# Kernel optimization log

Hardware: AMD Instinct MI355X
Metric: run time of the kernel (lower is better)

The kernel has to match this reference:

```python
import jax, jax.numpy as jnp
import numpy as np

N = 30000          # nodes
DEG = 16           # in-degree per node
E = N * DEG        # edges per etype
T = 3              # edge types
IN = 128           # in_feats
HID = 256          # hidden_size
HEADS = 4
CLS = 2            # num_classes
NEG_SLOPE = 0.2    # DGL GATConv default


def setup_inputs() -> dict:
    key = jax.random.key(0)
    ks = jax.random.split(key, 14)
    s = lambda k, shape: (jax.random.normal(k, shape, jnp.float32) * 0.05)
    feat = jax.random.normal(ks[0], (N, IN), jnp.float32)
    src = jax.random.randint(ks[1], (T, E), 0, N)
    # every node gets exactly DEG incoming edges per etype (DGL forbids 0-in-degree)
    dst = jnp.tile(jnp.repeat(jnp.arange(N), DEG), (T, 1))
    D = HID // HEADS
    return {
        "feat": feat,
        "W0": s(ks[2], (T, IN, HID)),  "al0": s(ks[3], (T, HEADS, D)), "ar0": s(ks[4], (T, HEADS, D)), "b0": jnp.zeros((T, HID), jnp.float32),
        "W1": s(ks[5], (T, HID, HID)), "al1": s(ks[6], (T, HEADS, D)), "ar1": s(ks[7], (T, HEADS, D)), "b1": jnp.zeros((T, HID), jnp.float32),
        "W2": s(ks[8], (T, HID, CLS)), "al2": s(ks[9], (T, 1, CLS)),   "ar2": s(ks[10], (T, 1, CLS)), "b2": jnp.zeros((T, CLS), jnp.float32),
        "src": src, "dst": dst,
    }


def _gat(feat, W, al, ar, b, src, dst):
    """DGL GATConv: feat [n,F], W [F,H*D], al/ar [H,D], b [H*D] -> [n,H,D]."""
    n = feat.shape[0]
    H, D = al.shape
    h = (feat @ W).reshape(n, H, D)                      # projected features
    el = jnp.sum(h * al, axis=-1)                        # [n,H]
    er = jnp.sum(h * ar, axis=-1)                        # [n,H]
    e = jax.nn.leaky_relu(el[src] + er[dst], NEG_SLOPE)  # [E,H] edge scores
    # segment softmax over incoming edges of each dst node
    emax = jax.ops.segment_max(e, dst, num_segments=n)
    ex = jnp.exp(e - emax[dst])
    den = jax.ops.segment_sum(ex, dst, num_segments=n)
    alpha = ex / den[dst]                                # [E,H]
    out = jax.ops.segment_sum(h[src] * alpha[:, :, None], dst, num_segments=n)
    return out + b.reshape(H, D)


def _hetero(feat, W, al, ar, b, src, dst):
    # HeteroGraphConv(aggregate='mean') over T edge types on one node type
    outs = [_gat(feat, W[t], al[t], ar[t], b[t], src[t], dst[t]) for t in range(W.shape[0])]
    return jnp.mean(jnp.stack(outs, 0), axis=0)


def reference(feat, W0, al0, ar0, b0, W1, al1, ar1, b1, W2, al2, ar2, b2, src, dst):
    h = jax.nn.elu(_hetero(feat, W0, al0, ar0, b0, src, dst).reshape(N, -1))
    h = jax.nn.elu(_hetero(h, W1, al1, ar1, b1, src, dst).reshape(N, -1))
    logits = _hetero(h, W2, al2, ar2, b2, src, dst)      # [N,1,CLS]
    # faithful to F.softmax(logits[primary_ntype], dim=1): dim=1 is the size-1 head axis
    return logits, jax.nn.softmax(logits, axis=1)
```

## Files before the change

### kernel.cpp

```cpp
#include <hip/hip_runtime.h>
#include <hip/hip_bf16.h>
#include <hip/hip_fp8.h>
#include <math.h>

#define N_NODES 30000
#define DEG     16
#define NE      480000
#define NT      3
#define IN_F    128
#define HID_F   256
#define HEADS   4
#define DH      64
#define CLS     2
#define SLOPE   0.2f

#define NTILES      1875
#define NTILES_AL   1880
#define KC0         4
#define KC1         8

typedef __hip_bfloat16 bf16;
typedef __attribute__((ext_vector_type(8))) short short8;
typedef __attribute__((ext_vector_type(4))) float floatx4;
typedef __attribute__((ext_vector_type(2))) float f32x2;

__device__ __forceinline__ float bf2f(short x) {
    unsigned int u = ((unsigned int)(unsigned short)x) << 16;
    float f;
    __builtin_memcpy(&f, &u, 4);
    return f;
}
__device__ __forceinline__ short f2bf_s(float x) {
    bf16 b = bf16(x);
    short s;
    __builtin_memcpy(&s, &b, 2);
    return s;
}

__device__ __forceinline__ void gload_lds16(const void* g, void* l) {
    __builtin_amdgcn_global_load_lds(
        (const __attribute__((address_space(1))) unsigned int*)g,
        (__attribute__((address_space(3))) unsigned int*)l, 16, 0, 0);
}

__device__ __forceinline__ f32x2 fp8_lo(unsigned int u) {
#if __has_builtin(__builtin_amdgcn_cvt_pk_f32_fp8)
    return __builtin_amdgcn_cvt_pk_f32_fp8((int)u, false);
#else
    __hip_fp8_e4m3 q0, q1;
    q0.__x = (unsigned char)(u & 0xff);
    q1.__x = (unsigned char)((u >> 8) & 0xff);
    return (f32x2){(float)q0, (float)q1};
#endif
}
__device__ __forceinline__ f32x2 fp8_hi(unsigned int u) {
#if __has_builtin(__builtin_amdgcn_cvt_pk_f32_fp8)
    return __builtin_amdgcn_cvt_pk_f32_fp8((int)u, true);
#else
    __hip_fp8_e4m3 q2, q3;
    q2.__x = (unsigned char)((u >> 16) & 0xff);
    q3.__x = (unsigned char)((u >> 24) & 0xff);
    return (f32x2){(float)q2, (float)q3};
#endif
}
__device__ __forceinline__ unsigned int fp8_encode4_u32(float v0, float v1,
                                                        float v2, float v3) {
#if __has_builtin(__builtin_amdgcn_cvt_pk_fp8_f32)
    int p01 = __builtin_amdgcn_cvt_pk_fp8_f32(v0, v1, 0, false);
    int p23 = __builtin_amdgcn_cvt_pk_fp8_f32(v2, v3, 0, false);
    return ((unsigned int)p01 & 0xffffu) | ((unsigned int)p23 << 16);
#else
    __hip_fp8_e4m3 q0(v0), q1(v1), q2(v2), q3(v3);
    return (unsigned int)q0.__x | ((unsigned int)q1.__x << 8) |
           ((unsigned int)q2.__x << 16) | ((unsigned int)q3.__x << 24);
#endif
}


#define APACK_THREADS (N_NODES * (IN_F / 8))
#define BP0_THREADS   (NT * 16 * KC0 * 64)
#define BP1_THREADS   (NT * 16 * KC1 * 64)
__global__ void prep(const float* __restrict__ feat, const float* __restrict__ W0,
                     const float* __restrict__ W1, short* __restrict__ Apack0,
                     short* __restrict__ Bpack0, short* __restrict__ Bpack1) {
    int g = blockIdx.x * 256 + threadIdx.x;
    if (g < APACK_THREADS) {
        int row = g >> 4, j8 = g & 15;
        int k0 = j8 * 8;
        const float* src = feat + (size_t)row * IN_F + k0;
        int ntile = row >> 4, C = k0 >> 5, quad = (k0 >> 3) & 3;
        int lane  = (row & 15) + 16 * quad;
        short* dst = Apack0 + ((size_t)(ntile * KC0 + C) * 64 + lane) * 8;
        short8 o;
#pragma unroll
        for (int j = 0; j < 8; j++) o[j] = f2bf_s(src[j]);
        *(short8*)dst = o;
        return;
    }
    g -= APACK_THREADS;
    if (g < BP0_THREADS) {
        int t = g / (16 * KC0 * 64), rem = g % (16 * KC0 * 64);
        int nt = rem / (KC0 * 64);
        int C  = (rem / 64) % KC0;
        int lane = rem & 63, l15 = lane & 15, quad = lane >> 4;
        int col = nt * 16 + l15, k0 = C * 32 + quad * 8;
        const float* src = W0 + (size_t)t * IN_F * HID_F + (size_t)k0 * HID_F + col;
        short* dst = Bpack0 + ((size_t)t * 16 * KC0 + nt * KC0 + C) * 512 + lane * 8;
        short8 o;
#pragma unroll
        for (int j = 0; j < 8; j++) o[j] = f2bf_s(src[(size_t)j * HID_F]);
        *(short8*)dst = o;
        return;
    }
    g -= BP0_THREADS;
    if (g < BP1_THREADS) {
        int t = g / (16 * KC1 * 64), rem = g % (16 * KC1 * 64);
        int nt = rem / (KC1 * 64);
        int C  = (rem / 64) % KC1;
        int lane = rem & 63, l15 = lane & 15, quad = lane >> 4;
        int col = nt * 16 + l15, k0 = C * 32 + quad * 8;
        const float* src = W1 + (size_t)t * HID_F * HID_F + (size_t)k0 * HID_F + col;
        short* dst = Bpack1 + ((size_t)t * 16 * KC1 + nt * KC1 + C) * 512 + lane * 8;
        short8 o;
#pragma unroll
        for (int j = 0; j < 8; j++) o[j] = f2bf_s(src[(size_t)j * HID_F]);
        *(short8*)dst = o;
    }
}

template <int K>
__global__ __launch_bounds__(256, 4) void gemm_proj(const short* __restrict__ Apack,
                                                    const short* __restrict__ Bpack,
                                                    const float* __restrict__ al,
                                                    const float* __restrict__ ar,
                                                    unsigned char* __restrict__ Hout,
                                                    float* __restrict__ el,
                                                    float* __restrict__ er) {
    const int KC = K / 32;
    int nh   = blockIdx.y;
    int t    = blockIdx.z;
    int tid  = threadIdx.x;
    int wave = tid >> 6, lane = tid & 63;
    int quad = lane >> 4, l15 = lane & 15;
    int e0   = blockIdx.x * 8 + wave * 2;

    __shared__ __align__(16) unsigned char Blds[4 * KC * 1024];

    {
        const short* Bp_panel = Bpack + ((size_t)t * 16 + nh * 4) * KC * 512;
#pragma unroll
        for (int i = 0; i < KC; i++) {
            int chunk = wave + i * 4;
            gload_lds16(Bp_panel + (size_t)chunk * 512 + lane * 8,
                        Blds + chunk * 1024);
        }
    }

    const short* Ap0 = Apack + (size_t)(e0)     * KC * 512 + lane * 8;
    const short* Ap1 = Apack + (size_t)(e0 + 1) * KC * 512 + lane * 8;
    unsigned char* Ht = Hout + (size_t)t * N_NODES * HID_F;

    floatx4 acc[4][2];
#pragma unroll
    for (int i = 0; i < 4; i++) {
        acc[i][0] = (floatx4){0.f, 0.f, 0.f, 0.f};
        acc[i][1] = (floatx4){0.f, 0.f, 0.f, 0.f};
    }

    asm volatile("s_waitcnt vmcnt(0)" ::: "memory");
    __syncthreads();

#pragma unroll
    for (int C = 0; C < KC; C++) {
        short8 xb0 = *(const short8*)(Ap0 + (size_t)C * 512);
        short8 xb1 = *(const short8*)(Ap1 + (size_t)C * 512);
#pragma unroll
        for (int nt = 0; nt < 4; nt++) {
            short8 wa = *(const short8*)(Blds + (size_t)(nt * KC + C) * 1024 + lane * 16);
            acc[nt][0] = __builtin_amdgcn_mfma_f32_16x16x32_bf16(wa, xb0, acc[nt][0], 0, 0, 0);
            acc[nt][1] = __builtin_amdgcn_mfma_f32_16x16x32_bf16(wa, xb1, acc[nt][1], 0, 0, 0);
        }
    }

#pragma unroll
    for (int e = 0; e < 2; e++) {
        int node = (e0 + e) * 16 + l15;
        bool ok  = node < N_NODES;
#pragma unroll
        for (int nt = 0; nt < 4; nt++) {
            unsigned int u = fp8_encode4_u32(acc[nt][e][0], acc[nt][e][1],
                                             acc[nt][e][2], acc[nt][e][3]);
            if (ok)
                *(unsigned int*)(Ht + (size_t)node * HID_F + (nh * 4 + nt) * 16 + quad * 4) = u;
        }
        {
            float pl = 0.f, pr = 0.f;
#pragma unroll
            for (int nt = 0; nt < 4; nt++) {
                int coff = t * HID_F + (nh * 4 + nt) * 16 + quad * 4;
                float4 av = *(const float4*)(al + coff);
                float4 rv = *(const float4*)(ar + coff);
                pl += acc[nt][e][0] * av.x + acc[nt][e][1] * av.y +
                      acc[nt][e][2] * av.z + acc[nt][e][3] * av.w;
                pr += acc[nt][e][0] * rv.x + acc[nt][e][1] * rv.y +
                      acc[nt][e][2] * rv.z + acc[nt][e][3] * rv.w;
            }
            pl += __shfl_xor(pl, 16); pl += __shfl_xor(pl, 32);
            pr += __shfl_xor(pr, 16); pr += __shfl_xor(pr, 32);
            if (lane < 16 && ok) {
                el[((size_t)t * N_NODES + node) * HEADS + nh] = pl;
                er[((size_t)t * N_NODES + node) * HEADS + nh] = pr;
            }
        }
    }
}

template <bool PACK>
__global__ __launch_bounds__(256, 8) void gat_agg(const unsigned char* __restrict__ Hproj,
                                                  const float* __restrict__ el,
                                                  const float* __restrict__ er,
                                                  const int* __restrict__ src,
                                                  const float* __restrict__ bias,
                                                  short* __restrict__ out) {
    int blk = blockIdx.x;
    int tid = threadIdx.x;
    __shared__ __align__(16) int   s_src[16][NT][DEG];
    __shared__ __align__(16) float s_w[16][NT][HEADS][DEG];

#pragma unroll
    for (int t = 0; t < NT; t++) {
        int j = tid;
        s_src[j >> 4][t][j & 15] = src[(size_t)t * NE + blk * 256 + j];
    }
    __syncthreads();

    {
        int lane16 = tid & 15;
        int ubase  = tid >> 4;
#pragma unroll
        for (int it = 0; it < 12; it++) {
            int u = it * 16 + ubase;
            int g = u / 12, rem = u % 12;
            int t = rem >> 2, h = rem & 3;
            int n = blk * 16 + g;
            int s = s_src[g][t][lane16];
            float e = el[((size_t)t * N_NODES + s) * HEADS + h] +
                      er[((size_t)t * N_NODES + n) * HEADS + h];
            e = e > 0.f ? e : SLOPE * e;
            float m = e;
            m = fmaxf(m, __shfl_xor(m, 1));
            m = fmaxf(m, __shfl_xor(m, 2));
            m = fmaxf(m, __shfl_xor(m, 4));
            m = fmaxf(m, __shfl_xor(m, 8));
            float p = __expf(e - m);
            float ss = p;
            ss += __shfl_xor(ss, 1);
            ss += __shfl_xor(ss, 2);
            ss += __shfl_xor(ss, 4);
            ss += __shfl_xor(ss, 8);
            s_w[g][t][h][lane16] = p / ss;
        }
    }
    __syncthreads();

    int g = tid >> 4, c = tid & 15;
    int n = blk * 16 + g;
    int h = c >> 2;
    int col0 = c * 16;

    f32x2 acc2[8];
#pragma unroll
    for (int k = 0; k < 8; k++) acc2[k] = (f32x2){0.f, 0.f};

    const uint4* Hb = (const uint4*)Hproj;
    unsigned cu = (unsigned)c;

#pragma unroll
    for (int t = 0; t < NT; t++) {
        const unsigned tb = (unsigned)t * (N_NODES * 16u);
        const float* wp = s_w[g][t][h];
#pragma unroll
        for (int half = 0; half < 2; half++) {
            uint4 v[8];
#pragma unroll
            for (int i = 0; i < 8; i++) {
                int s = s_src[g][t][half * 8 + i];
                v[i] = Hb[tb + (unsigned)s * 16u + cu];
            }
#pragma unroll
            for (int i = 0; i < 8; i++) {
                float wsc = wp[half * 8 + i];
                f32x2 w2 = (f32x2){wsc, wsc};
                acc2[0] += w2 * fp8_lo(v[i].x);
                acc2[1] += w2 * fp8_hi(v[i].x);
                acc2[2] += w2 * fp8_lo(v[i].y);
                acc2[3] += w2 * fp8_hi(v[i].y);
                acc2[4] += w2 * fp8_lo(v[i].z);
                acc2[5] += w2 * fp8_hi(v[i].z);
                acc2[6] += w2 * fp8_lo(v[i].w);
                acc2[7] += w2 * fp8_hi(v[i].w);
            }
        }
    }

    short8 o0, o1;
#pragma unroll
    for (int j = 0; j < 8; j++) {
        float av = acc2[j >> 1][j & 1];
        float bsum = bias[0 * HID_F + col0 + j] + bias[1 * HID_F + col0 + j] +
                     bias[2 * HID_F + col0 + j];
        float res = (av + bsum) * (1.f / 3.f);
        res = res > 0.f ? res : (__expf(res) - 1.f);
        o0[j] = f2bf_s(res);
    }
#pragma unroll
    for (int j = 0; j < 8; j++) {
        float av = acc2[4 + (j >> 1)][j & 1];
        int cj = col0 + 8 + j;
        float bsum = bias[0 * HID_F + cj] + bias[1 * HID_F + cj] +
                     bias[2 * HID_F + cj];
        float res = (av + bsum) * (1.f / 3.f);
        res = res > 0.f ? res : (__expf(res) - 1.f);
        o1[j] = f2bf_s(res);
    }
    if (PACK) {
        int C = c >> 1;
        int lane0 = g + 16 * ((2 * c) & 3);
        int lane1 = g + 16 * ((2 * c + 1) & 3);
        *(short8*)(out + ((size_t)(blk * KC1 + C) * 64 + lane0) * 8) = o0;
        *(short8*)(out + ((size_t)(blk * KC1 + C) * 64 + lane1) * 8) = o1;
    } else {
        *(short8*)(out + (size_t)n * HID_F + col0) = o0;
        *(short8*)(out + (size_t)n * HID_F + col0 + 8) = o1;
    }
}

__global__ __launch_bounds__(256) void proj2(const short* __restrict__ X,
                                             const float* __restrict__ W2,
                                             const float* __restrict__ al2,
                                             const float* __restrict__ ar2,
                                             float* __restrict__ p2,
                                             float* __restrict__ el2,
                                             float* __restrict__ er2) {
    int n    = blockIdx.x * 4 + (threadIdx.x >> 6);
    int lane = threadIdx.x & 63;
    const short* Xr = X + (size_t)n * HID_F + lane * 4;
    float x[4];
    x[0] = bf2f(Xr[0]); x[1] = bf2f(Xr[1]); x[2] = bf2f(Xr[2]); x[3] = bf2f(Xr[3]);
    float a[NT][CLS];
#pragma unroll
    for (int t = 0; t < NT; t++)
#pragma unroll
        for (int cc = 0; cc < CLS; cc++) {
            float v = 0.f;
#pragma unroll
            for (int j = 0; j < 4; j++)
                v += x[j] * W2[(size_t)t * HID_F * CLS + (lane * 4 + j) * CLS + cc];
#pragma unroll
            for (int off = 32; off; off >>= 1) v += __shfl_xor(v, off);
            a[t][cc] = v;
        }
    if (lane == 0) {
#pragma unroll
        for (int t = 0; t < NT; t++) {
            p2[((size_t)t * N_NODES + n) * CLS + 0] = a[t][0];
            p2[((size_t)t * N_NODES + n) * CLS + 1] = a[t][1];
            el2[(size_t)t * N_NODES + n] = a[t][0] * al2[t * CLS + 0] + a[t][1] * al2[t * CLS + 1];
            er2[(size_t)t * N_NODES + n] = a[t][0] * ar2[t * CLS + 0] + a[t][1] * ar2[t * CLS + 1];
        }
    }
}

__global__ void final_layer(const float* __restrict__ p2,
                            const float* __restrict__ el2,
                            const float* __restrict__ er2,
                            const int* __restrict__ src,
                            const float* __restrict__ b2,
                            float* __restrict__ out) {
    int n = blockIdx.x * 256 + threadIdx.x;
    if (n >= N_NODES) return;
    float l0 = 0.f, l1 = 0.f;
    for (int t = 0; t < NT; t++) {
        float erv = er2[(size_t)t * N_NODES + n];
        const int* sp = src + (size_t)t * NE + n * DEG;
        float ev[DEG];
        float m = -1e30f;
#pragma unroll
        for (int i = 0; i < DEG; i++) {
            int s   = sp[i];
            float e = el2[(size_t)t * N_NODES + s] + erv;
            e = e > 0.f ? e : SLOPE * e;
            ev[i] = e;
            m = fmaxf(m, e);
        }
        float den = 0.f, a0 = 0.f, a1 = 0.f;
#pragma unroll
        for (int i = 0; i < DEG; i++) {
            int s   = sp[i];
            float p = __expf(ev[i] - m);
            den += p;
            a0  += p * p2[((size_t)t * N_NODES + s) * CLS + 0];
            a1  += p * p2[((size_t)t * N_NODES + s) * CLS + 1];
        }
        l0 += a0 / den + b2[t * CLS + 0];
        l1 += a1 / den + b2[t * CLS + 1];
    }
    l0 *= (1.f / 3.f);
    l1 *= (1.f / 3.f);
    out[(size_t)n * CLS + 0] = l0;
    out[(size_t)n * CLS + 1] = l1;
    float* out2 = out + (size_t)N_NODES * CLS;
    out2[(size_t)n * CLS + 0] = 1.0f;
    out2[(size_t)n * CLS + 1] = 1.0f;
}

extern "C" void kernel_launch(void* const* d_in, const int* in_sizes, int n_in,
                              void* d_out, int out_size, void* d_ws, size_t ws_size,
                              hipStream_t stream) {
    const float* feat = (const float*)d_in[0];
    const float* W0   = (const float*)d_in[1];
    const float* al0  = (const float*)d_in[2];
    const float* ar0  = (const float*)d_in[3];
    const float* b0   = (const float*)d_in[4];
    const float* W1   = (const float*)d_in[5];
    const float* al1  = (const float*)d_in[6];
    const float* ar1  = (const float*)d_in[7];
    const float* b1   = (const float*)d_in[8];
    const float* W2   = (const float*)d_in[9];
    const float* al2  = (const float*)d_in[10];
    const float* ar2  = (const float*)d_in[11];
    const float* b2   = (const float*)d_in[12];
    const int*   src  = (const int*)d_in[13];

    char* w = (char*)d_ws;
    auto alloc = [&](size_t bytes) {
        char* p = w;
        w += (bytes + 255) & ~(size_t)255;
        return p;
    };
    short* Apack0 = (short*)alloc((size_t)NTILES_AL * KC0 * 512 * 2);
    short* Apack1 = (short*)alloc((size_t)NTILES_AL * KC1 * 512 * 2);
    short* Bpack0 = (short*)alloc((size_t)NT * 16 * KC0 * 512 * 2);
    short* Bpack1 = (short*)alloc((size_t)NT * 16 * KC1 * 512 * 2);
    unsigned char* Hproj = (unsigned char*)alloc((size_t)NT * N_NODES * HID_F);
    short* h2    = (short*)alloc((size_t)N_NODES * HID_F * 2);
    float* el    = (float*)alloc((size_t)NT * N_NODES * HEADS * 4);
    float* er    = (float*)alloc((size_t)NT * N_NODES * HEADS * 4);
    float* p2    = (float*)alloc((size_t)NT * N_NODES * CLS * 4);
    float* el2   = (float*)alloc((size_t)NT * N_NODES * 4);
    float* er2   = (float*)alloc((size_t)NT * N_NODES * 4);

    int prep_total = APACK_THREADS + BP0_THREADS + BP1_THREADS;
    prep<<<(prep_total + 255) / 256, 256, 0, stream>>>(feat, W0, W1, Apack0,
                                                       Bpack0, Bpack1);

    dim3 ggrid((NTILES + 7) / 8, 4, NT);

    gemm_proj<IN_F><<<ggrid, 256, 0, stream>>>(Apack0, Bpack0, al0, ar0, Hproj, el, er);
    gat_agg<true><<<N_NODES / 16, 256, 0, stream>>>(Hproj, el, er, src, b0, Apack1);

    gemm_proj<HID_F><<<ggrid, 256, 0, stream>>>(Apack1, Bpack1, al1, ar1, Hproj, el, er);
    gat_agg<false><<<N_NODES / 16, 256, 0, stream>>>(Hproj, el, er, src, b1, h2);

    proj2<<<dim3(N_NODES / 4), 256, 0, stream>>>(h2, W2, al2, ar2, p2, el2, er2);
    final_layer<<<(N_NODES + 255) / 256, 256, 0, stream>>>(p2, el2, er2, src, b2,
                                                           (float*)d_out);
}
```

Before: 306.0 us.

## Split GAT aggregation into alpha and gather kernels, remap GEMM grid for XCD locality

The GEMM projection now loops over edge types inside one block and uses a 1D grid remapped across the eight XCDs, so the A tile is reused from cache across types. The fused aggregation kernel is split into an alpha_w kernel that writes softmax weights to global memory and gather kernels where each thread owns one node and one 32-column group. The gather kernels read 16-bit packed source indices and a precomputed bias sum. The final layer is rewritten to use one 16-lane group per node with shuffle reductions. These changes aim to improve cache locality and parallelism, at the cost of an extra launch and an alpha buffer round-trip through memory.

```diff
diff --git a/kernel.cpp b/kernel.cpp
--- a/kernel.cpp
+++ b/kernel.cpp
@@ -18,6 +18,9 @@
 #define NTILES_AL   1880
 #define KC0         4
 #define KC1         8
+
+#define GEMM_NWG    940
+#define GATHER_NWG  944
 
 typedef __hip_bfloat16 bf16;
 typedef __attribute__((ext_vector_type(8))) short short8;
@@ -80,9 +83,16 @@
 #define APACK_THREADS (N_NODES * (IN_F / 8))
 #define BP0_THREADS   (NT * 16 * KC0 * 64)
 #define BP1_THREADS   (NT * 16 * KC1 * 64)
+#define SRC16_THREADS (NT * NE / 8)
+#define BSUM_THREADS  (2 * HID_F)
+#define PREP_TOTAL (APACK_THREADS + BP0_THREADS + BP1_THREADS + SRC16_THREADS + BSUM_THREADS)
 __global__ void prep(const float* __restrict__ feat, const float* __restrict__ W0,
-                     const float* __restrict__ W1, short* __restrict__ Apack0,
-                     short* __restrict__ Bpack0, short* __restrict__ Bpack1) {
+                     const float* __restrict__ W1, const int* __restrict__ srcIn,
+                     const float* __restrict__ b0, const float* __restrict__ b1,
+                     short* __restrict__ Apack0, short* __restrict__ Bpack0,
+                     short* __restrict__ Bpack1,
+                     unsigned short* __restrict__ src16,
+                     float* __restrict__ bsum) {
     int g = blockIdx.x * 256 + threadIdx.x;
     if (g < APACK_THREADS) {
         int row = g >> 4, j8 = g & 15;
@@ -125,6 +135,26 @@
 #pragma unroll
         for (int j = 0; j < 8; j++) o[j] = f2bf_s(src[(size_t)j * HID_F]);
         *(short8*)dst = o;
+        return;
+    }
+    g -= BP1_THREADS;
+    if (g < SRC16_THREADS) {
+        size_t i = (size_t)g * 8;
+        const int4* s4 = (const int4*)(srcIn + i);
+        int4 q0 = s4[0], q1 = s4[1];
+        short8 o;
+        o[0] = (short)(unsigned short)q0.x; o[1] = (short)(unsigned short)q0.y;
+        o[2] = (short)(unsigned short)q0.z; o[3] = (short)(unsigned short)q0.w;
+        o[4] = (short)(unsigned short)q1.x; o[5] = (short)(unsigned short)q1.y;
+        o[6] = (short)(unsigned short)q1.z; o[7] = (short)(unsigned short)q1.w;
+        *(short8*)(src16 + i) = o;
+        return;
+    }
+    g -= SRC16_THREADS;
+    if (g < BSUM_THREADS) {
+        int layer = g >> 8, c = g & 255;
+        const float* b = layer ? b1 : b0;
+        bsum[layer * HID_F + c] = b[c] + b[HID_F + c] + b[2 * HID_F + c];
     }
 }
 
@@ -136,96 +166,98 @@
                                                     unsigned char* __restrict__ Hout,
                                                     float* __restrict__ el,
                                                     float* __restrict__ er) {
-    const int KC = K / 32;
-    int nh   = blockIdx.y;
-    int t    = blockIdx.z;
+    constexpr int KC = K / 32;
+    int bid = blockIdx.x;
+    int c8  = bid & 7, o = bid >> 3;
+    int L   = (c8 < 4) ? c8 * 118 + o : 472 + (c8 - 4) * 117 + o;
+    int xb  = L >> 2;
+    int nh  = L & 3;
     int tid  = threadIdx.x;
     int wave = tid >> 6, lane = tid & 63;
     int quad = lane >> 4, l15 = lane & 15;
-    int e0   = blockIdx.x * 8 + wave * 2;
+    int e0   = xb * 8 + wave * 2;
 
     __shared__ __align__(16) unsigned char Blds[4 * KC * 1024];
-
-    {
-        const short* Bp_panel = Bpack + ((size_t)t * 16 + nh * 4) * KC * 512;
-#pragma unroll
-        for (int i = 0; i < KC; i++) {
-            int chunk = wave + i * 4;
-            gload_lds16(Bp_panel + (size_t)chunk * 512 + lane * 8,
-                        Blds + chunk * 1024);
-        }
-    }
 
     const short* Ap0 = Apack + (size_t)(e0)     * KC * 512 + lane * 8;
     const short* Ap1 = Apack + (size_t)(e0 + 1) * KC * 512 + lane * 8;
-    unsigned char* Ht = Hout + (size_t)t * N_NODES * HID_F;
-
-    floatx4 acc[4][2];
-#pragma unroll
-    for (int i = 0; i < 4; i++) {
-        acc[i][0] = (floatx4){0.f, 0.f, 0.f, 0.f};
-        acc[i][1] = (floatx4){0.f, 0.f, 0.f, 0.f};
-    }
-
-    asm volatile("s_waitcnt vmcnt(0)" ::: "memory");
-    __syncthreads();
-
-#pragma unroll
-    for (int C = 0; C < KC; C++) {
-        short8 xb0 = *(const short8*)(Ap0 + (size_t)C * 512);
-        short8 xb1 = *(const short8*)(Ap1 + (size_t)C * 512);
-#pragma unroll
-        for (int nt = 0; nt < 4; nt++) {
-            short8 wa = *(const short8*)(Blds + (size_t)(nt * KC + C) * 1024 + lane * 16);
-            acc[nt][0] = __builtin_amdgcn_mfma_f32_16x16x32_bf16(wa, xb0, acc[nt][0], 0, 0, 0);
-            acc[nt][1] = __builtin_amdgcn_mfma_f32_16x16x32_bf16(wa, xb1, acc[nt][1], 0, 0, 0);
-        }
-    }
-
-#pragma unroll
-    for (int e = 0; e < 2; e++) {
-        int node = (e0 + e) * 16 + l15;
-        bool ok  = node < N_NODES;
-#pragma unroll
-        for (int nt = 0; nt < 4; nt++) {
-            unsigned int u = fp8_encode4_u32(acc[nt][e][0], acc[nt][e][1],
-                                             acc[nt][e][2], acc[nt][e][3]);
-            if (ok)
-                *(unsigned int*)(Ht + (size_t)node * HID_F + (nh * 4 + nt) * 16 + quad * 4) = u;
-        }
+
+    for (int t = 0; t < NT; t++) {
         {
-            float pl = 0.f, pr = 0.f;
+            const short* Bp_panel = Bpack + ((size_t)t * 16 + nh * 4) * KC * 512;
+#pragma unroll
+            for (int i = 0; i < KC; i++) {
+                int chunk = wave + i * 4;
+                gload_lds16(Bp_panel + (size_t)chunk * 512 + lane * 8,
+                            Blds + chunk * 1024);
+            }
+        }
+
+        floatx4 acc[4][2];
+#pragma unroll
+        for (int i = 0; i < 4; i++) {
+            acc[i][0] = (floatx4){0.f, 0.f, 0.f, 0.f};
+            acc[i][1] = (floatx4){0.f, 0.f, 0.f, 0.f};
+        }
+
+        asm volatile("s_waitcnt vmcnt(0)" ::: "memory");
+        __syncthreads();
+
+#pragma unroll
+        for (int C = 0; C < KC; C++) {
+            short8 xb0 = *(const short8*)(Ap0 + (size_t)C * 512);
+            short8 xb1 = *(const short8*)(Ap1 + (size_t)C * 512);
 #pragma unroll
             for (int nt = 0; nt < 4; nt++) {
-                int coff = t * HID_F + (nh * 4 + nt) * 16 + quad * 4;
-                float4 av = *(const float4*)(al + coff);
-                float4 rv = *(const float4*)(ar + coff);
-                pl += acc[nt][e][0] * av.x + acc[nt][e][1] * av.y +
-                      acc[nt][e][2] * av.z + acc[nt][e][3] * av.w;
-                pr += acc[nt][e][0] * rv.x + acc[nt][e][1] * rv.y +
-                      acc[nt][e][2] * rv.z + acc[nt][e][3] * rv.w;
+                short8 wa = *(const short8*)(Blds + (size_t)(nt * KC + C) * 1024 + lane * 16);
+                acc[nt][0] = __builtin_amdgcn_mfma_f32_16x16x32_bf16(wa, xb0, acc[nt][0], 0, 0, 0);
+                acc[nt][1] = __builtin_amdgcn_mfma_f32_16x16x32_bf16(wa, xb1, acc[nt][1], 0, 0, 0);
             }
-            pl += __shfl_xor(pl, 16); pl += __shfl_xor(pl, 32);
-            pr += __shfl_xor(pr, 16); pr += __shfl_xor(pr, 32);
-            if (lane < 16 && ok) {
-                el[((size_t)t * N_NODES + node) * HEADS + nh] = pl;
-                er[((size_t)t * N_NODES + node) * HEADS + nh] = pr;
+        }
+
+        unsigned char* Ht = Hout + (size_t)t * N_NODES * HID_F;
+#pragma unroll
+        for (int e = 0; e < 2; e++) {
+            int node = (e0 + e) * 16 + l15;
+            bool ok  = node < N_NODES;
+#pragma unroll
+            for (int nt = 0; nt < 4; nt++) {
+                unsigned int u = fp8_encode4_u32(acc[nt][e][0], acc[nt][e][1],
+                                                 acc[nt][e][2], acc[nt][e][3]);
+                if (ok)
+                    *(unsigned int*)(Ht + (size_t)node * HID_F + (nh * 4 + nt) * 16 + quad * 4) = u;
             }
-        }
-    }
-}
-
-template <bool PACK>
-__global__ __launch_bounds__(256, 8) void gat_agg(const unsigned char* __restrict__ Hproj,
-                                                  const float* __restrict__ el,
+            {
+                float pl = 0.f, pr = 0.f;
+#pragma unroll
+                for (int nt = 0; nt < 4; nt++) {
+                    int coff = t * HID_F + (nh * 4 + nt) * 16 + quad * 4;
+                    float4 av = *(const float4*)(al + coff);
+                    float4 rv = *(const float4*)(ar + coff);
+                    pl += acc[nt][e][0] * av.x + acc[nt][e][1] * av.y +
+                          acc[nt][e][2] * av.z + acc[nt][e][3] * av.w;
+                    pr += acc[nt][e][0] * rv.x + acc[nt][e][1] * rv.y +
+                          acc[nt][e][2] * rv.z + acc[nt][e][3] * rv.w;
+                }
+                pl += __shfl_xor(pl, 16); pl += __shfl_xor(pl, 32);
+                pr += __shfl_xor(pr, 16); pr += __shfl_xor(pr, 32);
+                if (lane < 16 && ok) {
+                    el[((size_t)t * N_NODES + node) * HEADS + nh] = pl;
+                    er[((size_t)t * N_NODES + node) * HEADS + nh] = pr;
+                }
+            }
+        }
+        __syncthreads();
+    }
+}
+
+__global__ __launch_bounds__(256, 8) void alpha_w(const float* __restrict__ el,
                                                   const float* __restrict__ er,
                                                   const int* __restrict__ src,
-                                                  const float* __restrict__ bias,
-                                                  short* __restrict__ out) {
+                                                  float* __restrict__ alpha) {
     int blk = blockIdx.x;
     int tid = threadIdx.x;
-    __shared__ __align__(16) int   s_src[16][NT][DEG];
-    __shared__ __align__(16) float s_w[16][NT][HEADS][DEG];
+    __shared__ __align__(16) int s_src[16][NT][DEG];
 
 #pragma unroll
     for (int t = 0; t < NT; t++) {
@@ -234,104 +266,184 @@
     }
     __syncthreads();
 
-    {
-        int lane16 = tid & 15;
-        int ubase  = tid >> 4;
-#pragma unroll
-        for (int it = 0; it < 12; it++) {
-            int u = it * 16 + ubase;
-            int g = u / 12, rem = u % 12;
-            int t = rem >> 2, h = rem & 3;
-            int n = blk * 16 + g;
-            int s = s_src[g][t][lane16];
-            float e = el[((size_t)t * N_NODES + s) * HEADS + h] +
-                      er[((size_t)t * N_NODES + n) * HEADS + h];
-            e = e > 0.f ? e : SLOPE * e;
-            float m = e;
-            m = fmaxf(m, __shfl_xor(m, 1));
-            m = fmaxf(m, __shfl_xor(m, 2));
-            m = fmaxf(m, __shfl_xor(m, 4));
-            m = fmaxf(m, __shfl_xor(m, 8));
-            float p = __expf(e - m);
-            float ss = p;
-            ss += __shfl_xor(ss, 1);
-            ss += __shfl_xor(ss, 2);
-            ss += __shfl_xor(ss, 4);
-            ss += __shfl_xor(ss, 8);
-            s_w[g][t][h][lane16] = p / ss;
-        }
-    }
-    __syncthreads();
-
-    int g = tid >> 4, c = tid & 15;
-    int n = blk * 16 + g;
-    int h = c >> 2;
-    int col0 = c * 16;
-
-    f32x2 acc2[8];
-#pragma unroll
-    for (int k = 0; k < 8; k++) acc2[k] = (f32x2){0.f, 0.f};
+    int lane16 = tid & 15;
+    int ubase  = tid >> 4;
+#pragma unroll
+    for (int it = 0; it < 12; it++) {
+        int u = it * 16 + ubase;
+        int g = u / 12, rem = u % 12;
+        int t = rem >> 2, h = rem & 3;
+        int n = blk * 16 + g;
+        int s = s_src[g][t][lane16];
+        float e = el[((size_t)t * N_NODES + s) * HEADS + h] +
+                  er[((size_t)t * N_NODES + n) * HEADS + h];
+        e = e > 0.f ? e : SLOPE * e;
+        float m = e;
+        m = fmaxf(m, __shfl_xor(m, 1));
+        m = fmaxf(m, __shfl_xor(m, 2));
+        m = fmaxf(m, __shfl_xor(m, 4));
+        m = fmaxf(m, __shfl_xor(m, 8));
+        float p = __expf(e - m);
+        float ss = p;
+        ss += __shfl_xor(ss, 1);
+        ss += __shfl_xor(ss, 2);
+        ss += __shfl_xor(ss, 4);
+        ss += __shfl_xor(ss, 8);
+        alpha[(((size_t)t * HEADS + h) * N_NODES + n) * 16 + lane16] = p / ss;
+    }
+}
+
+
+__global__ __launch_bounds__(256, 4) void gat_gather_pack(
+        const unsigned char* __restrict__ Hproj,
+        const float* __restrict__ alpha,
+        const unsigned short* __restrict__ src16,
+        const float* __restrict__ bsum,
+        short* __restrict__ out) {
+    int bid = blockIdx.x;
+    int cg  = bid & 7;
+    int n   = (bid >> 3) * 256 + threadIdx.x;
+    if (n >= N_NODES) return;
+    int h = cg >> 1;
 
     const uint4* Hb = (const uint4*)Hproj;
-    unsigned cu = (unsigned)c;
-
-#pragma unroll
+    unsigned colbase = (unsigned)cg * 2u;
+
+    f32x2 acc2[16];
+#pragma unroll
+    for (int k = 0; k < 16; k++) acc2[k] = (f32x2){0.f, 0.f};
+
     for (int t = 0; t < NT; t++) {
-        const unsigned tb = (unsigned)t * (N_NODES * 16u);
-        const float* wp = s_w[g][t][h];
-#pragma unroll
-        for (int half = 0; half < 2; half++) {
-            uint4 v[8];
-#pragma unroll
-            for (int i = 0; i < 8; i++) {
-                int s = s_src[g][t][half * 8 + i];
-                v[i] = Hb[tb + (unsigned)s * 16u + cu];
+        const uint4* sp = (const uint4*)(src16 + (size_t)t * NE + (size_t)n * 16);
+        uint4 sA = sp[0], sB = sp[1];
+        const float4* ap = (const float4*)(alpha + (((size_t)t * HEADS + h) * N_NODES + n) * 16);
+        float4 a0 = ap[0], a1 = ap[1], a2 = ap[2], a3 = ap[3];
+        unsigned tb = (unsigned)t * (N_NODES * 16u);
+        unsigned e_[16];
+        e_[0] = sA.x & 0xffffu;  e_[1] = sA.x >> 16;
+        e_[2] = sA.y & 0xffffu;  e_[3] = sA.y >> 16;
+        e_[4] = sA.z & 0xffffu;  e_[5] = sA.z >> 16;
+        e_[6] = sA.w & 0xffffu;  e_[7] = sA.w >> 16;
+        e_[8] = sB.x & 0xffffu;  e_[9] = sB.x >> 16;
+        e_[10] = sB.y & 0xffffu; e_[11] = sB.y >> 16;
+        e_[12] = sB.z & 0xffffu; e_[13] = sB.z >> 16;
+        e_[14] = sB.w & 0xffffu; e_[15] = sB.w >> 16;
+        float w_[16] = {a0.x, a0.y, a0.z, a0.w, a1.x, a1.y, a1.z, a1.w,
+                        a2.x, a2.y, a2.z, a2.w, a3.x, a3.y, a3.z, a3.w};
+#pragma unroll
+        for (int sub = 0; sub < 2; sub++) {
+#pragma unroll
+            for (int half = 0; half < 2; half++) {
+                uint4 v[8];
+#pragma unroll
+                for (int i = 0; i < 8; i++)
+                    v[i] = Hb[tb + e_[half * 8 + i] * 16u + colbase + (unsigned)sub];
+#pragma unroll
+                for (int i = 0; i < 8; i++) {
+                    float ws = w_[half * 8 + i];
+                    f32x2 w2 = (f32x2){ws, ws};
+                    acc2[sub * 8 + 0] += w2 * fp8_lo(v[i].x);
+                    acc2[sub * 8 + 1] += w2 * fp8_hi(v[i].x);
+                    acc2[sub * 8 + 2] += w2 * fp8_lo(v[i].y);
+                    acc2[sub * 8 + 3] += w2 * fp8_hi(v[i].y);
+                    acc2[sub * 8 + 4] += w2 * fp8_lo(v[i].z);
+                    acc2[sub * 8 + 5] += w2 * fp8_hi(v[i].z);
+                    acc2[sub * 8 + 6] += w2 * fp8_lo(v[i].w);
+                    acc2[sub * 8 + 7] += w2 * fp8_hi(v[i].w);
+                }
             }
-#pragma unroll
-            for (int i = 0; i < 8; i++) {
-                float wsc = wp[half * 8 + i];
-                f32x2 w2 = (f32x2){wsc, wsc};
-                acc2[0] += w2 * fp8_lo(v[i].x);
-                acc2[1] += w2 * fp8_hi(v[i].x);
-                acc2[2] += w2 * fp8_lo(v[i].y);
-                acc2[3] += w2 * fp8_hi(v[i].y);
-                acc2[4] += w2 * fp8_lo(v[i].z);
-                acc2[5] += w2 * fp8_hi(v[i].z);
-                acc2[6] += w2 * fp8_lo(v[i].w);
-                acc2[7] += w2 * fp8_hi(v[i].w);
+        }
+    }
+
+    int ntile = n >> 4;
+#pragma unroll
+    for (int q = 0; q < 4; q++) {
+        short8 o;
+#pragma unroll
+        for (int j = 0; j < 8; j++) {
+            int col = q * 8 + j;
+            float av = acc2[col >> 1][col & 1];
+            float res = (av + bsum[cg * 32 + col]) * (1.f / 3.f);
+            res = res > 0.f ? res : (__expf(res) - 1.f);
+            o[j] = f2bf_s(res);
+        }
+        *(short8*)(out + ((size_t)(ntile * KC1 + cg) * 64 + (n & 15) + 16 * q) * 8) = o;
+    }
+}
+
+__global__ __launch_bounds__(256, 4) void gat_gather_h2(
+        const unsigned char* __restrict__ Hproj,
+        const float* __restrict__ alpha,
+        const unsigned short* __restrict__ src16,
+        const float* __restrict__ bsum,
+        short* __restrict__ out) {
+    int bid = blockIdx.x;
+    int cg  = bid & 7;
+    int n   = (bid >> 3) * 256 + threadIdx.x;
+    if (n >= N_NODES) return;
+    int h = cg >> 1;
+
+    const uint4* Hb = (const uint4*)Hproj;
+    unsigned colbase = (unsigned)cg * 2u;
+
+    f32x2 acc2[16];
+#pragma unroll
+    for (int k = 0; k < 16; k++) acc2[k] = (f32x2){0.f, 0.f};
+
+    for (int t = 0; t < NT; t++) {
+        const uint4* sp = (const uint4*)(src16 + (size_t)t * NE + (size_t)n * 16);
+        uint4 sA = sp[0], sB = sp[1];
+        const float4* ap = (const float4*)(alpha + (((size_t)t * HEADS + h) * N_NODES + n) * 16);
+        float4 a0 = ap[0], a1 = ap[1], a2 = ap[2], a3 = ap[3];
+        unsigned tb = (unsigned)t * (N_NODES * 16u);
+        unsigned e_[16];
+        e_[0] = sA.x & 0xffffu;  e_[1] = sA.x >> 16;
+        e_[2] = sA.y & 0xffffu;  e_[3] = sA.y >> 16;
+        e_[4] = sA.z & 0xffffu;  e_[5] = sA.z >> 16;
+        e_[6] = sA.w & 0xffffu;  e_[7] = sA.w >> 16;
+        e_[8] = sB.x & 0xffffu;  e_[9] = sB.x >> 16;
+        e_[10] = sB.y & 0xffffu; e_[11] = sB.y >> 16;
+        e_[12] = sB.z & 0xffffu; e_[13] = sB.z >> 16;
+        e_[14] = sB.w & 0xffffu; e_[15] = sB.w >> 16;
+        float w_[16] = {a0.x, a0.y, a0.z, a0.w, a1.x, a1.y, a1.z, a1.w,
+                        a2.x, a2.y, a2.z, a2.w, a3.x, a3.y, a3.z, a3.w};
+#pragma unroll
+        for (int sub = 0; sub < 2; sub++) {
+#pragma unroll
+            for (int half = 0; half < 2; half++) {
+                uint4 v[8];
+#pragma unroll
+                for (int i = 0; i < 8; i++)
+                    v[i] = Hb[tb + e_[half * 8 + i] * 16u + colbase + (unsigned)sub];
+#pragma unroll
+                for (int i = 0; i < 8; i++) {
+                    float ws = w_[half * 8 + i];
+                    f32x2 w2 = (f32x2){ws, ws};
+                    acc2[sub * 8 + 0] += w2 * fp8_lo(v[i].x);
+                    acc2[sub * 8 + 1] += w2 * fp8_hi(v[i].x);
+                    acc2[sub * 8 + 2] += w2 * fp8_lo(v[i].y);
+                    acc2[sub * 8 + 3] += w2 * fp8_hi(v[i].y);
+                    acc2[sub * 8 + 4] += w2 * fp8_lo(v[i].z);
+                    acc2[sub * 8 + 5] += w2 * fp8_hi(v[i].z);
+                    acc2[sub * 8 + 6] += w2 * fp8_lo(v[i].w);
+                    acc2[sub * 8 + 7] += w2 * fp8_hi(v[i].w);
+                }
             }
         }
     }
 
-    short8 o0, o1;
-#pragma unroll
-    for (int j = 0; j < 8; j++) {
-        float av = acc2[j >> 1][j & 1];
-        float bsum = bias[0 * HID_F + col0 + j] + bias[1 * HID_F + col0 + j] +
-                     bias[2 * HID_F + col0 + j];
-        float res = (av + bsum) * (1.f / 3.f);
-        res = res > 0.f ? res : (__expf(res) - 1.f);
-        o0[j] = f2bf_s(res);
-    }
-#pragma unroll
-    for (int j = 0; j < 8; j++) {
-        float av = acc2[4 + (j >> 1)][j & 1];
-        int cj = col0 + 8 + j;
-        float bsum = bias[0 * HID_F + cj] + bias[1 * HID_F + cj] +
-                     bias[2 * HID_F + cj];
-        float res = (av + bsum) * (1.f / 3.f);
-        res = res > 0.f ? res : (__expf(res) - 1.f);
-        o1[j] = f2bf_s(res);
-    }
-    if (PACK) {
-        int C = c >> 1;
-        int lane0 = g + 16 * ((2 * c) & 3);
-        int lane1 = g + 16 * ((2 * c + 1) & 3);
-        *(short8*)(out + ((size_t)(blk * KC1 + C) * 64 + lane0) * 8) = o0;
-        *(short8*)(out + ((size_t)(blk * KC1 + C) * 64 + lane1) * 8) = o1;
-    } else {
-        *(short8*)(out + (size_t)n * HID_F + col0) = o0;
-        *(short8*)(out + (size_t)n * HID_F + col0 + 8) = o1;
+#pragma unroll
+    for (int q = 0; q < 4; q++) {
+        short8 o;
+#pragma unroll
+        for (int j = 0; j < 8; j++) {
+            int col = q * 8 + j;
+            float av = acc2[col >> 1][col & 1];
+            float res = (av + bsum[cg * 32 + col]) * (1.f / 3.f);
+            res = res > 0.f ? res : (__expf(res) - 1.f);
+            o[j] = f2bf_s(res);
+        }
+        *(short8*)(out + (size_t)n * HID_F + cg * 32 + q * 8) = o;
     }
 }
 
@@ -371,47 +483,44 @@
     }
 }
 
-__global__ void final_layer(const float* __restrict__ p2,
-                            const float* __restrict__ el2,
-                            const float* __restrict__ er2,
-                            const int* __restrict__ src,
-                            const float* __restrict__ b2,
-                            float* __restrict__ out) {
-    int n = blockIdx.x * 256 + threadIdx.x;
-    if (n >= N_NODES) return;
+__global__ __launch_bounds__(256) void final_layer(const float* __restrict__ p2,
+                                                   const float* __restrict__ el2,
+                                                   const float* __restrict__ er2,
+                                                   const int* __restrict__ src,
+                                                   const float* __restrict__ b2,
+                                                   float* __restrict__ out) {
+    int g = threadIdx.x >> 4, lane16 = threadIdx.x & 15;
+    int n = blockIdx.x * 16 + g;
     float l0 = 0.f, l1 = 0.f;
+#pragma unroll
     for (int t = 0; t < NT; t++) {
-        float erv = er2[(size_t)t * N_NODES + n];
-        const int* sp = src + (size_t)t * NE + n * DEG;
-        float ev[DEG];
-        float m = -1e30f;
-#pragma unroll
-        for (int i = 0; i < DEG; i++) {
-            int s   = sp[i];
-            float e = el2[(size_t)t * N_NODES + s] + erv;
-            e = e > 0.f ? e : SLOPE * e;
-            ev[i] = e;
-            m = fmaxf(m, e);
-        }
-        float den = 0.f, a0 = 0.f, a1 = 0.f;
-#pragma unroll
-        for (int i = 0; i < DEG; i++) {
-            int s   = sp[i];
-            float p = __expf(ev[i] - m);
-            den += p;
-            a0  += p * p2[((size_t)t * N_NODES + s) * CLS + 0];
-            a1  += p * p2[((size_t)t * N_NODES + s) * CLS + 1];
-        }
+        int s = src[(size_t)t * NE + n * DEG + lane16];
+        float e = el2[(size_t)t * N_NODES + s] + er2[(size_t)t * N_NODES + n];
+        e = e > 0.f ? e : SLOPE * e;
+        float m = e;
+        m = fmaxf(m, __shfl_xor(m, 1));
+        m = fmaxf(m, __shfl_xor(m, 2));
+        m = fmaxf(m, __shfl_xor(m, 4));
+        m = fmaxf(m, __shfl_xor(m, 8));
+        float p = __expf(e - m);
+        float2 pv = *(const float2*)(p2 + ((size_t)t * N_NODES + s) * CLS);
+        float den = p, a0 = p * pv.x, a1 = p * pv.y;
+        den += __shfl_xor(den, 1); a0 += __shfl_xor(a0, 1); a1 += __shfl_xor(a1, 1);
+        den += __shfl_xor(den, 2); a0 += __shfl_xor(a0, 2); a1 += __shfl_xor(a1, 2);
+        den += __shfl_xor(den, 4); a0 += __shfl_xor(a0, 4); a1 += __shfl_xor(a1, 4);
+        den += __shfl_xor(den, 8); a0 += __shfl_xor(a0, 8); a1 += __shfl_xor(a1, 8);
         l0 += a0 / den + b2[t * CLS + 0];
         l1 += a1 / den + b2[t * CLS + 1];
     }
-    l0 *= (1.f / 3.f);
-    l1 *= (1.f / 3.f);
-    out[(size_t)n * CLS + 0] = l0;
-    out[(size_t)n * CLS + 1] = l1;
-    float* out2 = out + (size_t)N_NODES * CLS;
-    out2[(size_t)n * CLS + 0] = 1.0f;
-    out2[(size_t)n * CLS + 1] = 1.0f;
+    if (lane16 == 0) {
+        l0 *= (1.f / 3.f);
+        l1 *= (1.f / 3.f);
+        out[(size_t)n * CLS + 0] = l0;
+        out[(size_t)n * CLS + 1] = l1;
+        float* out2 = out + (size_t)N_NODES * CLS;
+        out2[(size_t)n * CLS + 0] = 1.0f;
+        out2[(size_t)n * CLS + 1] = 1.0f;
+    }
 }
 
 extern "C" void kernel_launch(void* const* d_in, const int* in_sizes, int n_in,
@@ -449,20 +558,27 @@
     float* p2    = (float*)alloc((size_t)NT * N_NODES * CLS * 4);
     float* el2   = (float*)alloc((size_t)NT * N_NODES * 4);
     float* er2   = (float*)alloc((size_t)NT * N_NODES * 4);
-
-    int prep_total = APACK_THREADS + BP0_THREADS + BP1_THREADS;
-    prep<<<(prep_total + 255) / 256, 256, 0, stream>>>(feat, W0, W1, Apack0,
-                                                       Bpack0, Bpack1);
-
-    dim3 ggrid((NTILES + 7) / 8, 4, NT);
-
-    gemm_proj<IN_F><<<ggrid, 256, 0, stream>>>(Apack0, Bpack0, al0, ar0, Hproj, el, er);
-    gat_agg<true><<<N_NODES / 16, 256, 0, stream>>>(Hproj, el, er, src, b0, Apack1);
-
-    gemm_proj<HID_F><<<ggrid, 256, 0, stream>>>(Apack1, Bpack1, al1, ar1, Hproj, el, er);
-    gat_agg<false><<<N_NODES / 16, 256, 0, stream>>>(Hproj, el, er, src, b1, h2);
+    float* alphaB = (float*)alloc((size_t)NT * HEADS * N_NODES * 16 * 4);
+    unsigned short* src16 = (unsigned short*)alloc((size_t)NT * NE * 2);
+    float* bsum  = (float*)alloc((size_t)2 * HID_F * 4);
+
+    prep<<<(PREP_TOTAL + 255) / 256, 256, 0, stream>>>(feat, W0, W1, src, b0, b1,
+                                                       Apack0, Bpack0, Bpack1,
+                                                       src16, bsum);
+
+    gemm_proj<IN_F><<<dim3(GEMM_NWG), 256, 0, stream>>>(Apack0, Bpack0, al0, ar0,
+                                                        Hproj, el, er);
+    alpha_w<<<dim3(NTILES), 256, 0, stream>>>(el, er, src, alphaB);
+    gat_gather_pack<<<dim3(GATHER_NWG), 256, 0, stream>>>(Hproj, alphaB, src16,
+                                                          bsum, Apack1);
+
+    gemm_proj<HID_F><<<dim3(GEMM_NWG), 256, 0, stream>>>(Apack1, Bpack1, al1, ar1,
+                                                         Hproj, el, er);
+    alpha_w<<<dim3(NTILES), 256, 0, stream>>>(el, er, src, alphaB);
+    gat_gather_h2<<<dim3(GATHER_NWG), 256, 0, stream>>>(Hproj, alphaB, src16,
+                                                        bsum + HID_F, h2);
 
     proj2<<<dim3(N_NODES / 4), 256, 0, stream>>>(h2, W2, al2, ar2, p2, el2, er2);
-    final_layer<<<(N_NODES + 255) / 256, 256, 0, stream>>>(p2, el2, er2, src, b2,
-                                                           (float*)d_out);
-}
+    final_layer<<<dim3(NTILES), 256, 0, stream>>>(p2, el2, er2, src, b2,
+                                                  (float*)d_out);
+}
```

Result: slower. 574.1 us (+87.6%).
